# Performance work log

Hardware: AMD Instinct MI355X
Metric: run time of the kernel (lower is better)

The kernel has to match this reference:

```python
import jax, jax.numpy as jnp
import numpy as np
import math

D_MODEL = 1024
NUM_HEADS = 16
HEAD_DIM = D_MODEL // NUM_HEADS
ROPE_BASE = 10000.0
ROTARY_DIM = HEAD_DIM - HEAD_DIM % 2  # 64


def setup_inputs() -> dict:
    key = jax.random.key(0)
    ks = jax.random.split(key, 6)
    B, T = 4, 2048
    tokens = jax.random.normal(ks[0], (B, T, D_MODEL), dtype=jnp.float32)
    padding_mask = jax.random.randint(ks[1], (B, T), 0, 2) == 1  # True = pad
    s = 1.0 / math.sqrt(D_MODEL)
    W_qkv = jax.random.normal(ks[2], (D_MODEL, 3 * D_MODEL), dtype=jnp.float32) * s
    b_qkv = jnp.zeros((3 * D_MODEL,), dtype=jnp.float32)
    W_out = jax.random.normal(ks[3], (D_MODEL, D_MODEL), dtype=jnp.float32) * s
    b_out = jnp.zeros((D_MODEL,), dtype=jnp.float32)
    return {"tokens": tokens, "padding_mask": padding_mask,
            "W_qkv": W_qkv, "b_qkv": b_qkv, "W_out": W_out, "b_out": b_out}


def _apply_rope(x):
    # x: [B, H, T, head_dim]; full head dim is rotary here (ROTARY_DIM == HEAD_DIM)
    T = x.shape[-2]
    pos = jnp.arange(T, dtype=jnp.float32)[:, None]                      # [T,1]
    freqs = jnp.exp(jnp.arange(0, ROTARY_DIM, 2, dtype=jnp.float32)
                    * (-math.log(ROPE_BASE) / ROTARY_DIM))               # [rd/2]
    ang = pos * freqs[None, :]                                           # [T, rd/2]
    sin = jnp.sin(ang)[None, None].astype(x.dtype)
    cos = jnp.cos(ang)[None, None].astype(x.dtype)
    rot = x[..., :ROTARY_DIM].reshape(*x.shape[:-1], ROTARY_DIM // 2, 2)
    even, odd = rot[..., 0], rot[..., 1]
    rotated = jnp.stack((even * cos - odd * sin, even * sin + odd * cos), axis=-1)
    rotated = rotated.reshape(*x.shape[:-1], ROTARY_DIM)
    return jnp.concatenate([rotated, x[..., ROTARY_DIM:]], axis=-1)


def _safe_key_padding_mask(padding_mask):
    # True = pad; if a row is fully padded, unmask it to avoid NaN softmax rows
    all_pad = jnp.all(padding_mask, axis=-1, keepdims=True)
    return jnp.where(all_pad, False, padding_mask)


def reference(tokens, padding_mask, W_qkv, b_qkv, W_out, b_out):
    B, T, _ = tokens.shape
    qkv = tokens @ W_qkv + b_qkv                                         # [B,T,3d]
    q, k, v = jnp.split(qkv, 3, axis=-1)
    def split_heads(x):
        return x.reshape(B, T, NUM_HEADS, HEAD_DIM).transpose(0, 2, 1, 3)
    q, k, v = split_heads(q), split_heads(k), split_heads(v)
    q = _apply_rope(q)
    k = _apply_rope(k)
    valid = ~_safe_key_padding_mask(padding_mask)                        # [B,T], True = attend
    scores = jnp.einsum('bhqd,bhkd->bhqk', q, k) / math.sqrt(HEAD_DIM)   # [B,H,T,T]
    neg = jnp.asarray(jnp.finfo(scores.dtype).min, scores.dtype)
    scores = jnp.where(valid[:, None, None, :], scores, neg)
    attn = jax.nn.softmax(scores, axis=-1)
    out = jnp.einsum('bhqk,bhkd->bhqd', attn, v)                         # [B,H,T,hd]
    out = out.transpose(0, 2, 1, 3).reshape(B, T, D_MODEL)
    return out @ W_out + b_out
```

## Files before the change

kernel.cpp:

```cpp
#include <hip/hip_runtime.h>
#include <cmath>

#define T_SEQ 2048
#define NH    16
#define HD    64
#define DM    1024
#define BATCH 4

typedef __attribute__((ext_vector_type(8))) short s16x8;
typedef __attribute__((ext_vector_type(8))) _Float16 f16x8;
typedef __attribute__((ext_vector_type(2))) __fp16 fp16v2;
typedef __attribute__((ext_vector_type(4))) float f32x4;
typedef unsigned short ushort_t;

__device__ __forceinline__ ushort_t f2h(float x) {
    union { _Float16 h; ushort_t u; } v; v.h = (_Float16)x; return v.u;
}
__device__ __forceinline__ float h2f(ushort_t u) {
    union { ushort_t u; _Float16 h; } v; v.u = u; return (float)v.h;
}
__device__ __forceinline__ float exp2_raw(float x) {
    return __builtin_amdgcn_exp2f(x);
}
__device__ __forceinline__ unsigned pkrtz(float a, float b) {
    union { fp16v2 h; unsigned u; } v;
    v.h = __builtin_amdgcn_cvt_pkrtz(a, b);
    return v.u;
}

__device__ __forceinline__ void dma16(const void* g, const void* l) {
    __builtin_amdgcn_global_load_lds(
        (const __attribute__((address_space(1))) unsigned int*)(unsigned long long)g,
        (__attribute__((address_space(3))) unsigned int*)(unsigned int)(unsigned long long)l,
        16, 0, 0);
}

__global__ void maskprep_kernel(const int* __restrict__ pad, float* __restrict__ valid)
{
    __shared__ int sall[256];
    const int b = blockIdx.x;
    const int t = threadIdx.x;
    int allp = 1;
    for (int i = t; i < T_SEQ; i += 256) allp &= (pad[b*T_SEQ + i] != 0) ? 1 : 0;
    sall[t] = allp;
    __syncthreads();
    for (int s = 128; s > 0; s >>= 1) {
        if (t < s) sall[t] &= sall[t + s];
        __syncthreads();
    }
    const int ap = sall[0];
    for (int i = t; i < T_SEQ; i += 256) {
        const int p = (pad[b*T_SEQ + i] != 0) ? 1 : 0;
        valid[b*T_SEQ + i] = (p && !ap) ? -1e30f : 0.0f;
    }
}

__global__ __launch_bounds__(256)
void transpose_h_kernel(const float* __restrict__ W,
                        ushort_t* __restrict__ Th, int K, int N)
{
    __shared__ float T[64][68];
    const int tid = threadIdx.x;
    const int n0 = blockIdx.x * 64;
    const int k0 = blockIdx.y * 64;
#pragma unroll
    for (int i = 0; i < 4; ++i) {
        const int kr = (tid >> 4) + i*16;
        const int nc = (tid & 15) * 4;
        const float4 v = *(const float4*)&W[(size_t)(k0 + kr)*N + n0 + nc];
        T[nc+0][kr] = v.x; T[nc+1][kr] = v.y; T[nc+2][kr] = v.z; T[nc+3][kr] = v.w;
    }
    __syncthreads();
#pragma unroll
    for (int i = 0; i < 4; ++i) {
        const int nr = (tid >> 4) + i*16;
        const int kc = (tid & 15) * 4;
        ushort_t h[4];
#pragma unroll
        for (int j = 0; j < 4; ++j) h[j] = f2h(T[nr][kc + j] * 32.0f);
        const size_t off = (size_t)(n0 + nr)*K + k0 + kc;
        *(short4*)&Th[off] = make_short4((short)h[0], (short)h[1], (short)h[2], (short)h[3]);
    }
}

__global__ __launch_bounds__(256)
void split_kernel(const float* __restrict__ X, ushort_t* __restrict__ H)
{
    const int i = blockIdx.x * 256 + threadIdx.x;
    const float4 v = ((const float4*)X)[i];
    *(short4*)&H[(size_t)i*4] = make_short4(
        (short)f2h(v.x), (short)f2h(v.y), (short)f2h(v.z), (short)f2h(v.w));
}

template<int EPI>
__global__ __launch_bounds__(256)
void mfma_gemm_kernel(const ushort_t* __restrict__ Atf,
                      const ushort_t* __restrict__ BTh,
                      const float* __restrict__ bias,
                      float* __restrict__ O0,
                      ushort_t* __restrict__ Qf,
                      ushort_t* __restrict__ Khf,
                      ushort_t* __restrict__ Vthf,
                      int M, int N, int K)
{
    __shared__ __align__(16) char smem[34816];
    char* smA0 = smem;
    char* smA1 = smem + 4096;
    char* smB0 = smem + 8192;
    char* smB1 = smem + 16384;

    const int tid  = threadIdx.x;
    const int w    = tid >> 6;
    const int ln   = tid & 63;
    const int lx   = ln & 15;
    const int quad = ln >> 4;
    const int mw   = (w >> 1) * 32;
    const int nw   = (w & 1) * 64;
    const int m0   = blockIdx.y * 64;
    const int n0   = blockIdx.x * 128;

    const int swc = ((ln & 3) ^ ((ln >> 3) & 3)) * 8;
    const size_t gaA = (size_t)(m0 + w*16 + (ln >> 2))*K + swc;
    const size_t gaB = (size_t)(n0 + w*32 + (ln >> 2))*K + swc;
    const int ldsA = (w*64 + ln)*16;
    const int ldsB = (w*128 + ln)*16;

#define ISSUE_DMA(kk, dA, dB) do {                                       \
        dma16(Atf + gaA + (kk),        (dA) + ldsA);                     \
        dma16(BTh + gaB + (kk),        (dB) + ldsB);                     \
        dma16(BTh + gaB + 16*K + (kk), (dB) + ldsB + 1024);              \
    } while (0)

    f32x4 acc[2][4];
#pragma unroll
    for (int mt = 0; mt < 2; ++mt)
#pragma unroll
        for (int nt = 0; nt < 4; ++nt) acc[mt][nt] = (f32x4){0.f,0.f,0.f,0.f};

    const int cs = (quad ^ ((lx >> 1) & 3)) * 16;

#define GEMM_STEP(kk, cA, cB, nA, nB) do {                                \
        if ((kk) + 32 < K) ISSUE_DMA((kk) + 32, nA, nB);                  \
        f16x8 bfh[4];                                                     \
        _Pragma("unroll")                                                 \
        for (int nt = 0; nt < 4; ++nt)                                    \
            bfh[nt] = *(const f16x8*)((cB) + (nw + nt*16 + lx)*64 + cs);  \
        const f16x8 af0 = *(const f16x8*)((cA) + (mw + lx)*64 + cs);      \
        const f16x8 af1 = *(const f16x8*)((cA) + (mw + 16 + lx)*64 + cs); \
        __builtin_amdgcn_s_setprio(1);                                    \
        _Pragma("unroll")                                                 \
        for (int nt = 0; nt < 4; ++nt) {                                  \
            acc[0][nt] = __builtin_amdgcn_mfma_f32_16x16x32_f16(af0, bfh[nt], acc[0][nt], 0, 0, 0); \
            acc[1][nt] = __builtin_amdgcn_mfma_f32_16x16x32_f16(af1, bfh[nt], acc[1][nt], 0, 0, 0); \
        }                                                                 \
        __builtin_amdgcn_s_setprio(0);                                    \
        __syncthreads();                                                  \
    } while (0)

    ISSUE_DMA(0, smA0, smB0);
    __syncthreads();
    for (int kk = 0; kk < K; kk += 64) {
        GEMM_STEP(kk,      smA0, smB0, smA1, smB1);
        GEMM_STEP(kk + 32, smA1, smB1, smA0, smB0);
    }
#undef GEMM_STEP
#undef ISSUE_DMA

    const float INV32 = 0.03125f;
    if (EPI == 0) {
#pragma unroll
        for (int nt = 0; nt < 4; ++nt) {
            const int n = n0 + nw + nt*16 + lx;
#pragma unroll
            for (int mt = 0; mt < 2; ++mt)
#pragma unroll
                for (int r = 0; r < 4; ++r) {
                    const int m = m0 + mw + mt*16 + quad*4 + r;
                    O0[(size_t)m*N + n] = acc[mt][nt][r]*INV32 + bias[n];
                }
        }
    } else {
        const int which = n0 >> 10;
        const int hbase = (n0 & 1023) >> 6;
        const int b     = m0 >> 11;
        const int t0    = m0 & 2047;
        float* Ct = (float*)smem;
        const float ssign = (lx & 1) ? 1.0f : -1.0f;

        __syncthreads();
        if (which < 2) {
#pragma unroll
            for (int nt = 0; nt < 4; ++nt) {
                const int nl = nw + nt*16 + lx;
                const int d  = nl & 63;
                const float bn = bias[n0 + nl];
                const float freq = expf(-(float)(d >> 1) * 0.28782313662425575f);
#pragma unroll
                for (int mt = 0; mt < 2; ++mt)
#pragma unroll
                    for (int r = 0; r < 4; ++r) {
                        const int ml = mw + mt*16 + quad*4 + r;
                        const int t  = t0 + ml;
                        float res = acc[mt][nt][r]*INV32 + bn;
                        const float ang = (float)t * freq;
                        const float sn = sinf(ang), cs2 = cosf(ang);
                        const float prt = __shfl_xor(res, 1);
                        res = res*cs2 + ssign*prt*sn;
                        if (which == 0) res *= 0.18033688011112042f;
                        Ct[ml*132 + nl] = res;
                    }
            }
        } else {
#pragma unroll
            for (int nt = 0; nt < 4; ++nt) {
                const int nl = nw + nt*16 + lx;
                const float bn = bias[n0 + nl];
#pragma unroll
                for (int mt = 0; mt < 2; ++mt)
#pragma unroll
                    for (int r = 0; r < 4; ++r) {
                        const int ml = mw + mt*16 + quad*4 + r;
                        Ct[nl*68 + ml] = acc[mt][nt][r]*INV32 + bn;
                    }
            }
        }
        __syncthreads();

        if (which < 2) {
#pragma unroll
            for (int u = 0; u < 4; ++u) {
                const int L  = u*32 + (tid >> 3);
                const int t  = L & 63;
                const int hl = L >> 6;
                const int dg = (tid & 7) * 8;
                const float* src = &Ct[t*132 + hl*64 + dg];
                float v[8];
                *(f32x4*)&v[0] = *(const f32x4*)src;
                *(f32x4*)&v[4] = *(const f32x4*)(src + 4);
                s16x8 h8;
#pragma unroll
                for (int j = 0; j < 8; ++j) h8[j] = (short)f2h(v[j]);
                const int bh = b*NH + hbase + hl;
                const size_t off = (((size_t)bh)*T_SEQ + t0 + t)*64 + dg;
                if (which == 0) *(s16x8*)&Qf [off] = h8;
                else            *(s16x8*)&Khf[off] = h8;
            }
        } else {
#pragma unroll
            for (int u = 0; u < 4; ++u) {
                const int row = u*32 + (tid >> 3);
                const int d   = row & 63;
                const int hl  = row >> 6;
                const int tg  = (tid & 7) * 8;
                const float* src = &Ct[row*68 + tg];
                float v[8];
                *(f32x4*)&v[0] = *(const f32x4*)src;
                *(f32x4*)&v[4] = *(const f32x4*)(src + 4);
                s16x8 h8;
#pragma unroll
                for (int j = 0; j < 8; ++j) h8[j] = (short)f2h(v[j]);
                const int bh = b*NH + hbase + hl;
                const size_t off = (((size_t)bh)*HD + d)*T_SEQ + t0 + tg;
                *(s16x8*)&Vthf[off] = h8;
            }
        }
    }
}

__global__ __launch_bounds__(256, 3)
void attn_mfma_kernel(const ushort_t* __restrict__ Qf,
                      const ushort_t* __restrict__ Khf,
                      const ushort_t* __restrict__ Vthf,
                      const float* __restrict__ mbias,
                      ushort_t* __restrict__ AOf)
{
    __shared__ ushort_t KH[64*64];
    __shared__ ushort_t VH[64*64];
    __shared__ float    MB[T_SEQ];

    const int tid  = threadIdx.x;
    const int w    = tid >> 6;
    const int ln   = tid & 63;
    const int lx   = ln & 15;
    const int quad = ln >> 4;

    const int id = blockIdx.x;
    const int qt = (id >> 3) & 15;
    const int bh = ((id >> 7) << 3) | (id & 7);
    const int b  = bh >> 4;
    const int h  = bh & 15;
    const int qrow0 = qt*128 + w*32;

    f16x8 qf[2][2];
#pragma unroll
    for (int qb = 0; qb < 2; ++qb) {
        const size_t qo = (((size_t)bh)*T_SEQ + qrow0 + qb*16 + lx)*HD + quad*8;
        qf[qb][0] = *(const f16x8*)&Qf[qo];
        qf[qb][1] = *(const f16x8*)&Qf[qo + 32];
    }

    {
        const f32x4* msrc = (const f32x4*)(mbias + (size_t)b*T_SEQ);
        f32x4* mdst = (f32x4*)MB;
#pragma unroll
        for (int i = 0; i < 2; ++i) mdst[tid + i*256] = msrc[tid + i*256];
    }

    const int sj   = ln >> 3;
    const int sch  = ln & 7;
    const int srow = w*16 + sj;
    const size_t kg0 = ((size_t)bh*T_SEQ + srow)*HD + sch*8;
    const size_t vg0 = ((size_t)bh*HD + srow)*T_SEQ + sch*8;
    const int lw0 = srow*64 + ((sch ^ (sj & 3)) << 3);
    const int lw1 = (srow + 8)*64 + ((sch ^ (sj & 3) ^ 4) << 3);

    const int r0  = ((lx >> 2) << 3) + (lx & 3);
    const int ka0 = r0*64 + ((quad ^ (lx & 7)) << 3);
    const int gv  = (lx & 3) ^ (((lx >> 3) & 1) << 2);
    const int va0 = lx*64 + ((quad ^ gv) << 3);

    f32x4 o[2][4];
#pragma unroll
    for (int qb = 0; qb < 2; ++qb)
#pragma unroll
        for (int nt = 0; nt < 4; ++nt) o[qb][nt] = (f32x4){0.f, 0.f, 0.f, 0.f};
    float mrun[2] = {-INFINITY, -INFINITY};
    float lrun[2] = {0.f, 0.f};

    s16x8 rkh0, rkh1, rvh0, rvh1;
    rkh0 = *(const s16x8*)&Khf [kg0];
    rkh1 = *(const s16x8*)&Khf [kg0 + (size_t)8*HD];
    rvh0 = *(const s16x8*)&Vthf[vg0];
    rvh1 = *(const s16x8*)&Vthf[vg0 + (size_t)8*T_SEQ];
    *(s16x8*)&KH[lw0] = rkh0;  *(s16x8*)&KH[lw1] = rkh1;
    *(s16x8*)&VH[lw0] = rvh0;  *(s16x8*)&VH[lw1] = rvh1;
    __syncthreads();

    for (int kt = 0; kt < T_SEQ/64; ++kt) {
        const int ktn = (kt+1 < T_SEQ/64) ? kt+1 : kt;
        const size_t kgt = kg0 + (size_t)ktn*64*HD;
        const size_t vgt = vg0 + ktn*64;
        rkh0 = *(const s16x8*)&Khf [kgt];
        rkh1 = *(const s16x8*)&Khf [kgt + (size_t)8*HD];
        rvh0 = *(const s16x8*)&Vthf[vgt];
        rvh1 = *(const s16x8*)&Vthf[vgt + (size_t)8*T_SEQ];

        f32x4 mb[4];
#pragma unroll
        for (int nt = 0; nt < 4; ++nt)
            mb[nt] = *(const f32x4*)&MB[kt*64 + (quad << 3) + ((nt >> 1) << 5) + ((nt & 1) << 2)];

        f32x4 s[2][4];
        __builtin_amdgcn_s_setprio(1);
#pragma unroll
        for (int nt = 0; nt < 4; ++nt) {
            const int a0 = ka0 + ((nt & 1) << 8) + ((nt >> 1) << 11);
            const f16x8 kh0 = *(const f16x8*)&KH[a0];
            const f16x8 kh1 = *(const f16x8*)&KH[a0 ^ 32];
            s[0][nt] = mb[nt];
            s[1][nt] = mb[nt];
            s[0][nt] = __builtin_amdgcn_mfma_f32_16x16x32_f16(kh0, qf[0][0], s[0][nt], 0, 0, 0);
            s[0][nt] = __builtin_amdgcn_mfma_f32_16x16x32_f16(kh1, qf[0][1], s[0][nt], 0, 0, 0);
            s[1][nt] = __builtin_amdgcn_mfma_f32_16x16x32_f16(kh0, qf[1][0], s[1][nt], 0, 0, 0);
            s[1][nt] = __builtin_amdgcn_mfma_f32_16x16x32_f16(kh1, qf[1][1], s[1][nt], 0, 0, 0);
        }
        __builtin_amdgcn_s_setprio(0);

        float mt[2];
#pragma unroll
        for (int qb = 0; qb < 2; ++qb) {
            const float m0q = fmaxf(fmaxf(s[qb][0][0], s[qb][0][1]), fmaxf(s[qb][0][2], s[qb][0][3]));
            const float m1q = fmaxf(fmaxf(s[qb][1][0], s[qb][1][1]), fmaxf(s[qb][1][2], s[qb][1][3]));
            const float m2q = fmaxf(fmaxf(s[qb][2][0], s[qb][2][1]), fmaxf(s[qb][2][2], s[qb][2][3]));
            const float m3q = fmaxf(fmaxf(s[qb][3][0], s[qb][3][1]), fmaxf(s[qb][3][2], s[qb][3][3]));
            float m = fmaxf(fmaxf(m0q, m1q), fmaxf(m2q, m3q));
            m = fmaxf(m, __shfl_xor(m, 16));
            m = fmaxf(m, __shfl_xor(m, 32));
            mt[qb] = m;
        }

        const bool stable = (mt[0] - mrun[0] <= 8.0f) && (mt[1] - mrun[1] <= 8.0f);
        if (!__all(stable)) {
#pragma unroll
            for (int qb = 0; qb < 2; ++qb) {
                const float mnew  = fmaxf(mrun[qb], mt[qb]);
                const float alpha = exp2_raw(mrun[qb] - mnew);
                mrun[qb] = mnew;
                lrun[qb] *= alpha;
                float ar[4];
#pragma unroll
                for (int r = 0; r < 4; ++r)
                    ar[r] = __shfl(alpha, (ln & 48) | ((quad << 2) + r));
#pragma unroll
                for (int nt = 0; nt < 4; ++nt)
#pragma unroll
                    for (int r = 0; r < 4; ++r) o[qb][nt][r] *= ar[r];
            }
        }

        union PU { unsigned u[4]; f16x8 v; };
        PU pf[2][2];
#pragma unroll
        for (int qb = 0; qb < 2; ++qb) {
            float lt = 0.f;
#pragma unroll
            for (int nt = 0; nt < 4; ++nt)
#pragma unroll
                for (int r = 0; r < 4; ++r) {
                    s[qb][nt][r] = exp2_raw(s[qb][nt][r] - mrun[qb]);
                    lt += s[qb][nt][r];
                }
            lrun[qb] += lt;

            pf[qb][0].u[0] = pkrtz(s[qb][0][0], s[qb][0][1]);
            pf[qb][0].u[1] = pkrtz(s[qb][0][2], s[qb][0][3]);
            pf[qb][0].u[2] = pkrtz(s[qb][1][0], s[qb][1][1]);
            pf[qb][0].u[3] = pkrtz(s[qb][1][2], s[qb][1][3]);
            pf[qb][1].u[0] = pkrtz(s[qb][2][0], s[qb][2][1]);
            pf[qb][1].u[1] = pkrtz(s[qb][2][2], s[qb][2][3]);
            pf[qb][1].u[2] = pkrtz(s[qb][3][0], s[qb][3][1]);
            pf[qb][1].u[3] = pkrtz(s[qb][3][2], s[qb][3][3]);
        }

        __builtin_amdgcn_s_setprio(1);
#pragma unroll
        for (int nt = 0; nt < 4; ++nt) {
            const int v0 = va0 + (nt << 10);
            const f16x8 vh0 = *(const f16x8*)&VH[v0];
            const f16x8 vh1 = *(const f16x8*)&VH[v0 ^ 32];
            o[0][nt] = __builtin_amdgcn_mfma_f32_16x16x32_f16(pf[0][0].v, vh0, o[0][nt], 0, 0, 0);
            o[0][nt] = __builtin_amdgcn_mfma_f32_16x16x32_f16(pf[0][1].v, vh1, o[0][nt], 0, 0, 0);
            o[1][nt] = __builtin_amdgcn_mfma_f32_16x16x32_f16(pf[1][0].v, vh0, o[1][nt], 0, 0, 0);
            o[1][nt] = __builtin_amdgcn_mfma_f32_16x16x32_f16(pf[1][1].v, vh1, o[1][nt], 0, 0, 0);
        }
        __builtin_amdgcn_s_setprio(0);

        __syncthreads();
        *(s16x8*)&KH[lw0] = rkh0;  *(s16x8*)&KH[lw1] = rkh1;
        *(s16x8*)&VH[lw0] = rvh0;  *(s16x8*)&VH[lw1] = rvh1;
        __syncthreads();
    }

#pragma unroll
    for (int qb = 0; qb < 2; ++qb) {
        lrun[qb] += __shfl_xor(lrun[qb], 16);
        lrun[qb] += __shfl_xor(lrun[qb], 32);
        const float linv = 1.0f / lrun[qb];
        float ir[4];
#pragma unroll
        for (int r = 0; r < 4; ++r)
            ir[r] = __shfl(linv, (ln & 48) | ((quad << 2) + r));
#pragma unroll
        for (int nt = 0; nt < 4; ++nt)
#pragma unroll
            for (int r = 0; r < 4; ++r) {
                const int t = qrow0 + qb*16 + quad*4 + r;
                const float res = o[qb][nt][r] * ir[r];
                const size_t off = (((size_t)b)*T_SEQ + t)*DM + h*HD + nt*16 + lx;
                AOf[off] = f2h(res);
            }
    }
}

extern "C" void kernel_launch(void* const* d_in, const int* in_sizes, int n_in,
                              void* d_out, int out_size, void* d_ws, size_t ws_size,
                              hipStream_t stream)
{
    const float* tokens = (const float*)d_in[0];
    const int*   pad    = (const int*)d_in[1];
    const float* Wqkv   = (const float*)d_in[2];
    const float* bqkv   = (const float*)d_in[3];
    const float* Wout   = (const float*)d_in[4];
    const float* bout   = (const float*)d_in[5];
    float* out = (float*)d_out;

    const size_t SZ = (size_t)8388608;
    ushort_t* U = (ushort_t*)d_ws;
    ushort_t* Qf   = U;
    ushort_t* Khf  = U + SZ;
    ushort_t* Vthf = U + 2*SZ;
    float* MSK = (float*)(U + 6*SZ);
    ushort_t* R   = (ushort_t*)(MSK + 8192);
    ushort_t* WqkvTh = R;
    ushort_t* AOf = R;
    ushort_t* TokF = (ushort_t*)d_out;
    ushort_t* WoutTh = Khf;

    maskprep_kernel<<<dim3(BATCH), dim3(256), 0, stream>>>(pad, MSK);
    split_kernel<<<dim3(8192), dim3(256), 0, stream>>>(tokens, TokF);
    transpose_h_kernel<<<dim3(48, 16), dim3(256), 0, stream>>>(
        Wqkv, WqkvTh, DM, 3*DM);
    mfma_gemm_kernel<1><<<dim3(24, 128), dim3(256), 0, stream>>>(
        TokF, WqkvTh, bqkv, nullptr,
        Qf, Khf, Vthf, BATCH*T_SEQ, 3*DM, DM);
    attn_mfma_kernel<<<dim3(1024), dim3(256), 0, stream>>>(
        Qf, Khf, Vthf, MSK, AOf);
    transpose_h_kernel<<<dim3(16, 16), dim3(256), 0, stream>>>(
        Wout, WoutTh, DM, DM);
    mfma_gemm_kernel<0><<<dim3(8, 128), dim3(256), 0, stream>>>(
        AOf, WoutTh, bout, out,
        nullptr, nullptr, nullptr, BATCH*T_SEQ, DM, DM);
}
```

Before: 331.4 us.

## Enlarge GEMM block tile to 128x128 with 4x4 MFMA tiles per wave

```diff
diff --git a/kernel.cpp b/kernel.cpp
--- a/kernel.cpp
+++ b/kernel.cpp
@@ -105,54 +105,55 @@
 {
     __shared__ __align__(16) char smem[34816];
     char* smA0 = smem;
-    char* smA1 = smem + 4096;
-    char* smB0 = smem + 8192;
-    char* smB1 = smem + 16384;
+    char* smA1 = smem + 8192;
+    char* smB0 = smem + 16384;
+    char* smB1 = smem + 24576;
 
     const int tid  = threadIdx.x;
     const int w    = tid >> 6;
     const int ln   = tid & 63;
     const int lx   = ln & 15;
     const int quad = ln >> 4;
-    const int mw   = (w >> 1) * 32;
+    const int mw   = (w >> 1) * 64;
     const int nw   = (w & 1) * 64;
-    const int m0   = blockIdx.y * 64;
+    const int m0   = blockIdx.y * 128;
     const int n0   = blockIdx.x * 128;
 
     const int swc = ((ln & 3) ^ ((ln >> 3) & 3)) * 8;
-    const size_t gaA = (size_t)(m0 + w*16 + (ln >> 2))*K + swc;
+    const size_t gaA = (size_t)(m0 + w*32 + (ln >> 2))*K + swc;
     const size_t gaB = (size_t)(n0 + w*32 + (ln >> 2))*K + swc;
-    const int ldsA = (w*64 + ln)*16;
-    const int ldsB = (w*128 + ln)*16;
+    const int ldsAB = (w*128 + ln)*16;
 
 #define ISSUE_DMA(kk, dA, dB) do {                                       \
-        dma16(Atf + gaA + (kk),        (dA) + ldsA);                     \
-        dma16(BTh + gaB + (kk),        (dB) + ldsB);                     \
-        dma16(BTh + gaB + 16*K + (kk), (dB) + ldsB + 1024);              \
+        dma16(Atf + gaA + (kk),        (dA) + ldsAB);                    \
+        dma16(Atf + gaA + 16*K + (kk), (dA) + ldsAB + 1024);             \
+        dma16(BTh + gaB + (kk),        (dB) + ldsAB);                    \
+        dma16(BTh + gaB + 16*K + (kk), (dB) + ldsAB + 1024);             \
     } while (0)
 
-    f32x4 acc[2][4];
-#pragma unroll
-    for (int mt = 0; mt < 2; ++mt)
-#pragma unroll
-        for (int nt = 0; nt < 4; ++nt) acc[mt][nt] = (f32x4){0.f,0.f,0.f,0.f};
+    f32x4 acc[4][4];
+#pragma unroll
+    for (int a = 0; a < 4; ++a)
+#pragma unroll
+        for (int b = 0; b < 4; ++b) acc[a][b] = (f32x4){0.f,0.f,0.f,0.f};
 
     const int cs = (quad ^ ((lx >> 1) & 3)) * 16;
 
 #define GEMM_STEP(kk, cA, cB, nA, nB) do {                                \
         if ((kk) + 32 < K) ISSUE_DMA((kk) + 32, nA, nB);                  \
-        f16x8 bfh[4];                                                     \
+        f16x8 afr[4], bfr[4];                                             \
         _Pragma("unroll")                                                 \
-        for (int nt = 0; nt < 4; ++nt)                                    \
-            bfh[nt] = *(const f16x8*)((cB) + (nw + nt*16 + lx)*64 + cs);  \
-        const f16x8 af0 = *(const f16x8*)((cA) + (mw + lx)*64 + cs);      \
-        const f16x8 af1 = *(const f16x8*)((cA) + (mw + 16 + lx)*64 + cs); \
+        for (int a = 0; a < 4; ++a)                                       \
+            afr[a] = *(const f16x8*)((cA) + (mw + a*16 + lx)*64 + cs);    \
+        _Pragma("unroll")                                                 \
+        for (int b = 0; b < 4; ++b)                                       \
+            bfr[b] = *(const f16x8*)((cB) + (nw + b*16 + lx)*64 + cs);    \
         __builtin_amdgcn_s_setprio(1);                                    \
         _Pragma("unroll")                                                 \
-        for (int nt = 0; nt < 4; ++nt) {                                  \
-            acc[0][nt] = __builtin_amdgcn_mfma_f32_16x16x32_f16(af0, bfh[nt], acc[0][nt], 0, 0, 0); \
-            acc[1][nt] = __builtin_amdgcn_mfma_f32_16x16x32_f16(af1, bfh[nt], acc[1][nt], 0, 0, 0); \
-        }                                                                 \
+        for (int a = 0; a < 4; ++a)                                       \
+            _Pragma("unroll")                                             \
+            for (int b = 0; b < 4; ++b)                                   \
+                acc[a][b] = __builtin_amdgcn_mfma_f32_16x16x32_f16(afr[a], bfr[b], acc[a][b], 0, 0, 0); \
         __builtin_amdgcn_s_setprio(0);                                    \
         __syncthreads();                                                  \
     } while (0)
@@ -169,100 +170,107 @@
     const float INV32 = 0.03125f;
     if (EPI == 0) {
 #pragma unroll
-        for (int nt = 0; nt < 4; ++nt) {
-            const int n = n0 + nw + nt*16 + lx;
-#pragma unroll
-            for (int mt = 0; mt < 2; ++mt)
+        for (int a = 0; a < 4; ++a)
+#pragma unroll
+            for (int b = 0; b < 4; ++b) {
+                const int n = n0 + nw + b*16 + lx;
 #pragma unroll
                 for (int r = 0; r < 4; ++r) {
-                    const int m = m0 + mw + mt*16 + quad*4 + r;
-                    O0[(size_t)m*N + n] = acc[mt][nt][r]*INV32 + bias[n];
+                    const int m = m0 + mw + a*16 + quad*4 + r;
+                    O0[(size_t)m*N + n] = acc[a][b][r]*INV32 + bias[n];
                 }
-        }
+            }
     } else {
         const int which = n0 >> 10;
         const int hbase = (n0 & 1023) >> 6;
-        const int b     = m0 >> 11;
+        const int bb    = m0 >> 11;
         const int t0    = m0 & 2047;
         float* Ct = (float*)smem;
         const float ssign = (lx & 1) ? 1.0f : -1.0f;
 
-        __syncthreads();
-        if (which < 2) {
-#pragma unroll
-            for (int nt = 0; nt < 4; ++nt) {
-                const int nl = nw + nt*16 + lx;
-                const int d  = nl & 63;
-                const float bn = bias[n0 + nl];
-                const float freq = expf(-(float)(d >> 1) * 0.28782313662425575f);
-#pragma unroll
-                for (int mt = 0; mt < 2; ++mt)
-#pragma unroll
-                    for (int r = 0; r < 4; ++r) {
-                        const int ml = mw + mt*16 + quad*4 + r;
-                        const int t  = t0 + ml;
-                        float res = acc[mt][nt][r]*INV32 + bn;
-                        const float ang = (float)t * freq;
-                        const float sn = sinf(ang), cs2 = cosf(ang);
-                        const float prt = __shfl_xor(res, 1);
-                        res = res*cs2 + ssign*prt*sn;
-                        if (which == 0) res *= 0.18033688011112042f;
-                        Ct[ml*132 + nl] = res;
+#pragma unroll
+        for (int hh = 0; hh < 2; ++hh) {
+            if (which < 2) {
+                if ((w >> 1) == hh) {
+#pragma unroll
+                    for (int b = 0; b < 4; ++b) {
+                        const int nl = nw + b*16 + lx;
+                        const int d  = nl & 63;
+                        const float bn = bias[n0 + nl];
+                        const float freq = expf(-(float)(d >> 1) * 0.28782313662425575f);
+#pragma unroll
+                        for (int a = 0; a < 4; ++a)
+#pragma unroll
+                            for (int r = 0; r < 4; ++r) {
+                                const int ml = a*16 + quad*4 + r;
+                                const int t  = t0 + hh*64 + ml;
+                                float res = acc[a][b][r]*INV32 + bn;
+                                const float ang = (float)t * freq;
+                                const float sn = sinf(ang), cs2 = cosf(ang);
+                                const float prt = __shfl_xor(res, 1);
+                                res = res*cs2 + ssign*prt*sn;
+                                if (which == 0) res *= 0.18033688011112042f;
+                                Ct[ml*132 + nl] = res;
+                            }
                     }
+                }
+            } else {
+                if ((w >> 1) == hh) {
+#pragma unroll
+                    for (int b = 0; b < 4; ++b) {
+                        const int nl = nw + b*16 + lx;
+                        const float bn = bias[n0 + nl];
+#pragma unroll
+                        for (int a = 0; a < 4; ++a)
+#pragma unroll
+                            for (int r = 0; r < 4; ++r) {
+                                const int ml = a*16 + quad*4 + r;
+                                Ct[nl*68 + ml] = acc[a][b][r]*INV32 + bn;
+                            }
+                    }
+                }
             }
-        } else {
-#pragma unroll
-            for (int nt = 0; nt < 4; ++nt) {
-                const int nl = nw + nt*16 + lx;
-                const float bn = bias[n0 + nl];
-#pragma unroll
-                for (int mt = 0; mt < 2; ++mt)
-#pragma unroll
-                    for (int r = 0; r < 4; ++r) {
-                        const int ml = mw + mt*16 + quad*4 + r;
-                        Ct[nl*68 + ml] = acc[mt][nt][r]*INV32 + bn;
-                    }
+            __syncthreads();
+
+            if (which < 2) {
+#pragma unroll
+                for (int u = 0; u < 4; ++u) {
+                    const int L  = u*32 + (tid >> 3);
+                    const int t  = L & 63;
+                    const int hl = L >> 6;
+                    const int dg = (tid & 7) * 8;
+                    const float* src = &Ct[t*132 + hl*64 + dg];
+                    float v[8];
+                    *(f32x4*)&v[0] = *(const f32x4*)src;
+                    *(f32x4*)&v[4] = *(const f32x4*)(src + 4);
+                    s16x8 h8;
+#pragma unroll
+                    for (int j = 0; j < 8; ++j) h8[j] = (short)f2h(v[j]);
+                    const int bh2 = bb*NH + hbase + hl;
+                    const size_t off = (((size_t)bh2)*T_SEQ + t0 + hh*64 + t)*64 + dg;
+                    if (which == 0) *(s16x8*)&Qf [off] = h8;
+                    else            *(s16x8*)&Khf[off] = h8;
+                }
+            } else {
+#pragma unroll
+                for (int u = 0; u < 4; ++u) {
+                    const int row = u*32 + (tid >> 3);
+                    const int d   = row & 63;
+                    const int hl  = row >> 6;
+                    const int tg  = (tid & 7) * 8;
+                    const float* src = &Ct[row*68 + tg];
+                    float v[8];
+                    *(f32x4*)&v[0] = *(const f32x4*)src;
+                    *(f32x4*)&v[4] = *(const f32x4*)(src + 4);
+                    s16x8 h8;
+#pragma unroll
+                    for (int j = 0; j < 8; ++j) h8[j] = (short)f2h(v[j]);
+                    const int bh2 = bb*NH + hbase + hl;
+                    const size_t off = (((size_t)bh2)*HD + d)*T_SEQ + t0 + hh*64 + tg;
+                    *(s16x8*)&Vthf[off] = h8;
+                }
             }
-        }
-        __syncthreads();
-
-        if (which < 2) {
-#pragma unroll
-            for (int u = 0; u < 4; ++u) {
-                const int L  = u*32 + (tid >> 3);
-                const int t  = L & 63;
-                const int hl = L >> 6;
-                const int dg = (tid & 7) * 8;
-                const float* src = &Ct[t*132 + hl*64 + dg];
-                float v[8];
-                *(f32x4*)&v[0] = *(const f32x4*)src;
-                *(f32x4*)&v[4] = *(const f32x4*)(src + 4);
-                s16x8 h8;
-#pragma unroll
-                for (int j = 0; j < 8; ++j) h8[j] = (short)f2h(v[j]);
-                const int bh = b*NH + hbase + hl;
-                const size_t off = (((size_t)bh)*T_SEQ + t0 + t)*64 + dg;
-                if (which == 0) *(s16x8*)&Qf [off] = h8;
-                else            *(s16x8*)&Khf[off] = h8;
-            }
-        } else {
-#pragma unroll
-            for (int u = 0; u < 4; ++u) {
-                const int row = u*32 + (tid >> 3);
-                const int d   = row & 63;
-                const int hl  = row >> 6;
-                const int tg  = (tid & 7) * 8;
-                const float* src = &Ct[row*68 + tg];
-                float v[8];
-                *(f32x4*)&v[0] = *(const f32x4*)src;
-                *(f32x4*)&v[4] = *(const f32x4*)(src + 4);
-                s16x8 h8;
-#pragma unroll
-                for (int j = 0; j < 8; ++j) h8[j] = (short)f2h(v[j]);
-                const int bh = b*NH + hbase + hl;
-                const size_t off = (((size_t)bh)*HD + d)*T_SEQ + t0 + tg;
-                *(s16x8*)&Vthf[off] = h8;
-            }
+            __syncthreads();
         }
     }
 }
@@ -490,14 +498,14 @@
     split_kernel<<<dim3(8192), dim3(256), 0, stream>>>(tokens, TokF);
     transpose_h_kernel<<<dim3(48, 16), dim3(256), 0, stream>>>(
         Wqkv, WqkvTh, DM, 3*DM);
-    mfma_gemm_kernel<1><<<dim3(24, 128), dim3(256), 0, stream>>>(
+    mfma_gemm_kernel<1><<<dim3(24, 64), dim3(256), 0, stream>>>(
         TokF, WqkvTh, bqkv, nullptr,
         Qf, Khf, Vthf, BATCH*T_SEQ, 3*DM, DM);
     attn_mfma_kernel<<<dim3(1024), dim3(256), 0, stream>>>(
         Qf, Khf, Vthf, MSK, AOf);
     transpose_h_kernel<<<dim3(16, 16), dim3(256), 0, stream>>>(
         Wout, WoutTh, DM, DM);
-    mfma_gemm_kernel<0><<<dim3(8, 128), dim3(256), 0, stream>>>(
+    mfma_gemm_kernel<0><<<dim3(8, 64), dim3(256), 0, stream>>>(
         AOf, WoutTh, bout, out,
         nullptr, nullptr, nullptr, BATCH*T_SEQ, DM, DM);
 }
```

After: 767.2 us. 2.32x slower.
